# Performance work log

Measured on AMD Instinct MI355X. Metric: run time of the kernel, lower is better.

Reference implementation:

```python
import jax, jax.numpy as jnp
import numpy as np

KERNEL_SIZE = 3  # matches init kwarg

def setup_inputs() -> dict:
    key = jax.random.key(0)
    k1, k2, k3, k4 = jax.random.split(key, 4)
    N, C, L, OUT = 32, 64, 2048, 128
    inp = jax.random.normal(k1, (N, C, L), dtype=jnp.float32)
    # adjacency-like dense matrix (tree adjacency may be sparse; dense here)
    m = jax.random.uniform(k2, (N, L, L), dtype=jnp.float32)
    W = jax.random.normal(k3, (OUT, KERNEL_SIZE * C), dtype=jnp.float32) * 0.05
    b = jax.random.normal(k4, (OUT,), dtype=jnp.float32)
    return {"input": inp, "m": m, "W": W, "b": b}

def reference(input, m, W, b):
    # propagate features over the tree adjacency kernel_size-1 times
    ys = [input]
    y = input
    for _ in range(KERNEL_SIZE - 1):
        y = jnp.matmul(y, m)          # (N, C, L) @ (N, L, L) -> (N, C, L)
        ys.append(y)
    cat = jnp.concatenate(ys, axis=1)  # (N, k*C, L)
    # 1x1 conv == channel projection
    out = jnp.einsum('oc,ncl->nol', W, cat) + b[None, :, None]
    return out
```

## Files before the change

kernel.cpp:

```cpp
#include <hip/hip_runtime.h>
#include <hip/hip_bf16.h>

#define NB   32
#define CH   64
#define LL   2048
#define OUTC 128

typedef float  f32x4  __attribute__((ext_vector_type(4)));
typedef short  s16x8  __attribute__((ext_vector_type(8)));
typedef short  s16x4  __attribute__((ext_vector_type(4)));
typedef unsigned short u16;

__device__ __forceinline__ u16 f2bf(float f) {
  unsigned int u = __builtin_bit_cast(unsigned int, f);
  u += 0x7FFFu + ((u >> 16) & 1u);
  return (u16)(u >> 16);
}

__device__ __forceinline__ s16x8 pack8c(const float* v) {
  s16x8 r;
#pragma unroll
  for (int j = 0; j < 8; j += 2) {
    __hip_bfloat162 h = __float22bfloat162_rn(make_float2(v[j], v[j + 1]));
    short2 s;
    __builtin_memcpy(&s, &h, sizeof(s));
    r[j] = s.x; r[j + 1] = s.y;
  }
  return r;
}

__device__ __forceinline__ s16x4 pack4c(const f32x4& v) {
  s16x4 r;
  __hip_bfloat162 h0 = __float22bfloat162_rn(make_float2(v[0], v[1]));
  __hip_bfloat162 h1 = __float22bfloat162_rn(make_float2(v[2], v[3]));
  short2 s0, s1;
  __builtin_memcpy(&s0, &h0, sizeof(s0));
  __builtin_memcpy(&s1, &h1, sizeof(s1));
  r[0] = s0.x; r[1] = s0.y; r[2] = s1.x; r[3] = s1.y;
  return r;
}

#define NX (NB * CH * LL)
#define NW (OUTC * 3 * CH)
__global__ __launch_bounds__(256)
void cvt_inputs(const float* __restrict__ x, const float* __restrict__ W,
                u16* __restrict__ xb, u16* __restrict__ Wb)
{
  const size_t t8 = ((size_t)blockIdx.x * 256 + threadIdx.x) * 8;
  if (t8 < NX) {
    float v[8];
    *(f32x4*)(v)     = *(const f32x4*)(x + t8);
    *(f32x4*)(v + 4) = *(const f32x4*)(x + t8 + 4);
    *(s16x8*)(xb + t8) = pack8c(v);
  } else if (t8 - NX < NW) {
    const size_t w8 = t8 - NX;
    float v[8];
    *(f32x4*)(v)     = *(const f32x4*)(W + w8);
    *(f32x4*)(v + 4) = *(const f32x4*)(W + w8 + 4);
    *(s16x8*)(Wb + w8) = pack8c(v);
  }
}

__global__ __launch_bounds__(256, 2)
void prop1_pack(const u16* __restrict__ xb, const float* __restrict__ m,
                u16* __restrict__ y1, u16* __restrict__ mP)
{
  __shared__ float smem[4][32 * 128];

  const int n    = blockIdx.x >> 4;
  const int lt   = blockIdx.x & 15;
  const int tid  = threadIdx.x;
  const int wave = tid >> 6;
  const int lane = tid & 63;
  const int l15  = lane & 15;
  const int g4   = lane >> 4;
  const int colb = lt * 128 + wave * 32;

  const float* mn   = m + (size_t)n * LL * LL + lt * 128;
  const float* gsrc = mn + (size_t)(wave * 8 + (lane >> 5)) * LL + (lane & 31) * 4;
  const u16*   ap   = xb + (size_t)n * CH * LL + (size_t)l15 * LL + g4 * 8;
  u16* q0 = mP + (((size_t)n * 64 * LL + colb + l15) * 4 + g4) * 8;
  u16* o  = y1 + (size_t)n * CH * LL + colb + l15;

  f32x4 acc[4][2];
#pragma unroll
  for (int f = 0; f < 4; ++f)
#pragma unroll
    for (int h = 0; h < 2; ++h)
#pragma unroll
      for (int r = 0; r < 4; ++r) acc[f][h][r] = 0.f;

  s16x8 aP[4], aQ[4];

#define ALOAD(R, KB)                                                          \
  { const u16* _ap = ap + (KB) * 32;                                          \
    _Pragma("unroll") for (int f = 0; f < 4; ++f)                             \
      R[f] = *(const s16x8*)(_ap + (size_t)(f * 16) * LL); }

#define GLOAD(BI, KB)                                                         \
  { float* _sb = smem[BI];                                                    \
    _Pragma("unroll") for (int i = 0; i < 4; ++i) {                           \
      const float* _g = gsrc + (size_t)((KB) * 32 + i * 2) * LL;              \
      __builtin_amdgcn_global_load_lds(                                       \
        (const __attribute__((address_space(1))) void*)_g,                    \
        (__attribute__((address_space(3))) void*)(_sb + (wave * 4 + i) * 256),\
        16, 0, 0); } }

  ALOAD(aP, 0)
  __builtin_amdgcn_sched_barrier(0);
  GLOAD(0, 0) GLOAD(1, 1) GLOAD(2, 2)
  __builtin_amdgcn_sched_barrier(0);
  asm volatile("s_waitcnt vmcnt(8)" ::: "memory");
  __builtin_amdgcn_s_barrier();
  __builtin_amdgcn_sched_barrier(0);

#define K1_STEP(KB, CUR, NXT, VN, LAST)                                       \
  {                                                                           \
    if (!(LAST)) {                                                            \
      ALOAD(NXT, ((KB) + 1 < 64 ? (KB) + 1 : 63))                             \
      __builtin_amdgcn_sched_barrier(0);                                      \
      GLOAD(((KB) + 3) & 3, ((KB) + 3 < 64 ? (KB) + 3 : 63))                  \
      __builtin_amdgcn_sched_barrier(0);                                      \
    }                                                                         \
    const float* _t = smem[(KB) & 3] + wave * 32 + l15;                       \
    float _bv0[8], _bv1[8];                                                   \
    _Pragma("unroll") for (int j = 0; j < 8; ++j) {                           \
      _bv0[j] = _t[(g4 * 8 + j) * 128];                                       \
      _bv1[j] = _t[(g4 * 8 + j) * 128 + 16];                                  \
    }                                                                         \
    s16x8 _b0 = pack8c(_bv0), _b1 = pack8c(_bv1);                             \
    u16* _q = q0 + (size_t)(KB) * 65536;                                      \
    *(s16x8*)(_q)       = _b0;                                                \
    *(s16x8*)(_q + 512) = _b1;                                                \
    _Pragma("unroll") for (int f = 0; f < 4; ++f) {                           \
      acc[f][0] = __builtin_amdgcn_mfma_f32_16x16x32_bf16(CUR[f], _b0, acc[f][0], 0, 0, 0); \
      acc[f][1] = __builtin_amdgcn_mfma_f32_16x16x32_bf16(CUR[f], _b1, acc[f][1], 0, 0, 0); \
    }                                                                         \
    if (!(LAST)) {                                                            \
      __builtin_amdgcn_sched_barrier(0);                                      \
      asm volatile("s_waitcnt vmcnt(" VN ")" ::: "memory");                   \
      __builtin_amdgcn_s_barrier();                                           \
      __builtin_amdgcn_sched_barrier(0);                                      \
    }                                                                         \
  }

  K1_STEP(0, aP, aQ, "14", false)
  K1_STEP(1, aQ, aP, "20", false)
#pragma unroll 1
  for (int kb = 2; kb < 62; kb += 2) {
    K1_STEP(kb,     aP, aQ, "22", false)
    K1_STEP(kb + 1, aQ, aP, "22", false)
  }
  K1_STEP(62, aP, aQ, "22", false)
  K1_STEP(63, aQ, aP, "0",  true)

#pragma unroll
  for (int f = 0; f < 4; ++f)
#pragma unroll
    for (int r = 0; r < 4; ++r) {
      const int row = f * 16 + g4 * 4 + r;
      o[(size_t)row * LL]      = f2bf(acc[f][0][r]);
      o[(size_t)row * LL + 16] = f2bf(acc[f][1][r]);
    }
}

__global__ __launch_bounds__(256, 2)
void prop2_proj(const u16* __restrict__ y1, const u16* __restrict__ mP,
                const u16* __restrict__ xb, const u16* __restrict__ Wb,
                const float* __restrict__ bias, float* __restrict__ out)
{
  __shared__ u16 yT[128 * 72];

  const int n    = blockIdx.x >> 4;
  const int lt   = blockIdx.x & 15;
  const int tid  = threadIdx.x;
  const int wave = tid >> 6;
  const int lane = tid & 63;
  const int l15  = lane & 15;
  const int g4   = lane >> 4;
  const int colb = lt * 128 + wave * 32;

  const u16* mq = mP + (((size_t)n * 64 * LL + colb + l15) * 4 + g4) * 8;
  const u16* ap = y1 + (size_t)n * CH * LL + (size_t)l15 * LL + g4 * 8;

  f32x4 acc[4][2];
#pragma unroll
  for (int f = 0; f < 4; ++f)
#pragma unroll
    for (int h = 0; h < 2; ++h)
#pragma unroll
      for (int r = 0; r < 4; ++r) acc[f][h][r] = 0.f;

  s16x8 bA0, bA1, bB0, bB1, aA[4], aB[4];

#define K2_LOAD(B0, B1, AV, KB)                                              \
  {                                                                          \
    const u16* _mq = mq + (size_t)(KB) * 65536;                              \
    B0 = *(const s16x8*)(_mq);                                               \
    B1 = *(const s16x8*)(_mq + 512);                                         \
    const u16* _ap = ap + (KB) * 32;                                         \
    _Pragma("unroll") for (int f = 0; f < 4; ++f)                            \
      AV[f] = *(const s16x8*)(_ap + (size_t)(f * 16) * LL);                  \
  }

#define K2_COMP(B0, B1, AV)                                                  \
  _Pragma("unroll") for (int f = 0; f < 4; ++f) {                            \
    acc[f][0] = __builtin_amdgcn_mfma_f32_16x16x32_bf16(AV[f], B0, acc[f][0], 0, 0, 0); \
    acc[f][1] = __builtin_amdgcn_mfma_f32_16x16x32_bf16(AV[f], B1, acc[f][1], 0, 0, 0); \
  }

  K2_LOAD(bA0, bA1, aA, 0)
#pragma unroll 1
  for (int kb = 0; kb < 64; kb += 2) {
    K2_LOAD(bB0, bB1, aB, kb + 1)
    K2_COMP(bA0, bA1, aA)
    if (kb + 2 < 64) K2_LOAD(bA0, bA1, aA, kb + 2)
    K2_COMP(bB0, bB1, aB)
  }

#pragma unroll
  for (int f = 0; f < 4; ++f)
#pragma unroll
    for (int h = 0; h < 2; ++h) {
      const int c = wave * 32 + l15 + 16 * h;
      *(s16x4*)(&yT[c * 72 + f * 16 + g4 * 4]) = pack4c(acc[f][h]);
    }
  __syncthreads();

  f32x4 acc2[8][2];
#pragma unroll
  for (int f = 0; f < 8; ++f)
#pragma unroll
    for (int h = 0; h < 2; ++h)
#pragma unroll
      for (int r = 0; r < 4; ++r) acc2[f][h][r] = 0.f;

  const size_t cb = (size_t)n * CH * LL + colb + l15;
  const u16* xp  = xb + cb + (size_t)(g4 * 8) * LL;
  const u16* y1p = y1 + cb + (size_t)(g4 * 8) * LL;
  const u16* wq  = Wb + (size_t)l15 * 192 + g4 * 8;

#pragma unroll
  for (int kc = 0; kc < 6; ++kc) {
    const int k0 = kc * 32;
    s16x8 b0, b1;
    if (kc < 4) {
      const u16* src = (kc < 2) ? (xp + (size_t)k0 * LL)
                                : (y1p + (size_t)(k0 - 64) * LL);
#pragma unroll
      for (int j = 0; j < 8; ++j) {
        b0[j] = (short)src[(size_t)j * LL];
        b1[j] = (short)src[(size_t)j * LL + 16];
      }
    } else {
      const int rb = (kc - 4) * 32 + g4 * 8;
      b0 = *(const s16x8*)(&yT[(wave * 32 + l15) * 72 + rb]);
      b1 = *(const s16x8*)(&yT[(wave * 32 + l15 + 16) * 72 + rb]);
    }
#pragma unroll
    for (int f = 0; f < 8; ++f) {
      s16x8 af = *(const s16x8*)(wq + (size_t)(f * 16) * 192 + k0);
      acc2[f][0] = __builtin_amdgcn_mfma_f32_16x16x32_bf16(af, b0, acc2[f][0], 0, 0, 0);
      acc2[f][1] = __builtin_amdgcn_mfma_f32_16x16x32_bf16(af, b1, acc2[f][1], 0, 0, 0);
    }
  }

  float* op = out + (size_t)n * OUTC * LL + colb + l15;
#pragma unroll
  for (int f = 0; f < 8; ++f)
#pragma unroll
    for (int r = 0; r < 4; ++r) {
      const int row = f * 16 + g4 * 4 + r;
      op[(size_t)row * LL]      = acc2[f][0][r] + bias[row];
      op[(size_t)row * LL + 16] = acc2[f][1][r] + bias[row];
    }
}

extern "C" void kernel_launch(void* const* d_in, const int* in_sizes, int n_in,
                              void* d_out, int out_size, void* d_ws, size_t ws_size,
                              hipStream_t stream)
{
  const float* x = (const float*)d_in[0];
  const float* m = (const float*)d_in[1];
  const float* W = (const float*)d_in[2];
  const float* b = (const float*)d_in[3];
  float* out = (float*)d_out;

  u16* y1 = (u16*)d_ws;
  u16* xb = y1 + (size_t)NB * CH * LL;
  u16* Wb = xb + (size_t)NB * CH * LL;
  u16* mP = (u16*)((char*)d_ws + (25u << 20));

  cvt_inputs<<<dim3(2060), dim3(256), 0, stream>>>(x, W, xb, Wb);
  prop1_pack<<<dim3(NB * 16), dim3(256), 0, stream>>>(xb, m, y1, mP);
  prop2_proj<<<dim3(NB * 16), dim3(256), 0, stream>>>(y1, mP, xb, Wb, b, out);
}
```

Baseline: 271.6 us.

## Split propagation kernels into single-wave blocks and drop workgroup barriers

Both propagation kernels now launch 64-thread, single-wave blocks over a grid four times larger. Each wave owns a 32-column tile with its own small LDS ring, so the per-step s_barrier and __syncthreads go away and waits use only vmcnt. The second kernel also moves from double to triple register buffering of its global loads, keeping more memory requests in flight. In exchange, the hand-tuned vmcnt values must now match the new per-step load and store counts exactly, and there are more, smaller blocks to schedule.

```diff
diff --git a/kernel.cpp b/kernel.cpp
--- a/kernel.cpp
+++ b/kernel.cpp
@@ -61,23 +61,21 @@
   }
 }
 
-__global__ __launch_bounds__(256, 2)
+__global__ __launch_bounds__(64)
 void prop1_pack(const u16* __restrict__ xb, const float* __restrict__ m,
                 u16* __restrict__ y1, u16* __restrict__ mP)
 {
-  __shared__ float smem[4][32 * 128];
-
-  const int n    = blockIdx.x >> 4;
-  const int lt   = blockIdx.x & 15;
-  const int tid  = threadIdx.x;
-  const int wave = tid >> 6;
-  const int lane = tid & 63;
+  __shared__ float smem[4][32 * 32];
+
+  const int n    = blockIdx.x >> 6;
+  const int lt   = blockIdx.x & 63;
+  const int lane = threadIdx.x;
   const int l15  = lane & 15;
   const int g4   = lane >> 4;
-  const int colb = lt * 128 + wave * 32;
-
-  const float* mn   = m + (size_t)n * LL * LL + lt * 128;
-  const float* gsrc = mn + (size_t)(wave * 8 + (lane >> 5)) * LL + (lane & 31) * 4;
+  const int colb = lt * 32;
+
+  const float* mn   = m + (size_t)n * LL * LL + colb;
+  const float* gsrc = mn + (size_t)(lane >> 3) * LL + (lane & 7) * 4;
   const u16*   ap   = xb + (size_t)n * CH * LL + (size_t)l15 * LL + g4 * 8;
   u16* q0 = mP + (((size_t)n * 64 * LL + colb + l15) * 4 + g4) * 8;
   u16* o  = y1 + (size_t)n * CH * LL + colb + l15;
@@ -100,18 +98,15 @@
 #define GLOAD(BI, KB)                                                         \
   { float* _sb = smem[BI];                                                    \
     _Pragma("unroll") for (int i = 0; i < 4; ++i) {                           \
-      const float* _g = gsrc + (size_t)((KB) * 32 + i * 2) * LL;              \
+      const float* _g = gsrc + (size_t)((KB) * 32 + i * 8) * LL;              \
       __builtin_amdgcn_global_load_lds(                                       \
         (const __attribute__((address_space(1))) void*)_g,                    \
-        (__attribute__((address_space(3))) void*)(_sb + (wave * 4 + i) * 256),\
+        (__attribute__((address_space(3))) void*)(_sb + i * 256),             \
         16, 0, 0); } }
 
   ALOAD(aP, 0)
   __builtin_amdgcn_sched_barrier(0);
   GLOAD(0, 0) GLOAD(1, 1) GLOAD(2, 2)
-  __builtin_amdgcn_sched_barrier(0);
-  asm volatile("s_waitcnt vmcnt(8)" ::: "memory");
-  __builtin_amdgcn_s_barrier();
   __builtin_amdgcn_sched_barrier(0);
 
 #define K1_STEP(KB, CUR, NXT, VN, LAST)                                       \
@@ -122,11 +117,13 @@
       GLOAD(((KB) + 3) & 3, ((KB) + 3 < 64 ? (KB) + 3 : 63))                  \
       __builtin_amdgcn_sched_barrier(0);                                      \
     }                                                                         \
-    const float* _t = smem[(KB) & 3] + wave * 32 + l15;                       \
+    asm volatile("s_waitcnt vmcnt(" VN ")" ::: "memory");                     \
+    __builtin_amdgcn_sched_barrier(0);                                        \
+    const float* _t = smem[(KB) & 3] + l15;                                   \
     float _bv0[8], _bv1[8];                                                   \
     _Pragma("unroll") for (int j = 0; j < 8; ++j) {                           \
-      _bv0[j] = _t[(g4 * 8 + j) * 128];                                       \
-      _bv1[j] = _t[(g4 * 8 + j) * 128 + 16];                                  \
+      _bv0[j] = _t[(g4 * 8 + j) * 32];                                        \
+      _bv1[j] = _t[(g4 * 8 + j) * 32 + 16];                                   \
     }                                                                         \
     s16x8 _b0 = pack8c(_bv0), _b1 = pack8c(_bv1);                             \
     u16* _q = q0 + (size_t)(KB) * 65536;                                      \
@@ -136,23 +133,17 @@
       acc[f][0] = __builtin_amdgcn_mfma_f32_16x16x32_bf16(CUR[f], _b0, acc[f][0], 0, 0, 0); \
       acc[f][1] = __builtin_amdgcn_mfma_f32_16x16x32_bf16(CUR[f], _b1, acc[f][1], 0, 0, 0); \
     }                                                                         \
-    if (!(LAST)) {                                                            \
-      __builtin_amdgcn_sched_barrier(0);                                      \
-      asm volatile("s_waitcnt vmcnt(" VN ")" ::: "memory");                   \
-      __builtin_amdgcn_s_barrier();                                           \
-      __builtin_amdgcn_sched_barrier(0);                                      \
-    }                                                                         \
-  }
-
-  K1_STEP(0, aP, aQ, "14", false)
-  K1_STEP(1, aQ, aP, "20", false)
+  }
+
+  K1_STEP(0, aP, aQ, "16", false)
+  K1_STEP(1, aQ, aP, "22", false)
+  K1_STEP(2, aP, aQ, "28", false)
 #pragma unroll 1
-  for (int kb = 2; kb < 62; kb += 2) {
-    K1_STEP(kb,     aP, aQ, "22", false)
-    K1_STEP(kb + 1, aQ, aP, "22", false)
-  }
-  K1_STEP(62, aP, aQ, "22", false)
-  K1_STEP(63, aQ, aP, "0",  true)
+  for (int kb = 3; kb < 63; kb += 2) {
+    K1_STEP(kb,     aQ, aP, "30", false)
+    K1_STEP(kb + 1, aP, aQ, "30", false)
+  }
+  K1_STEP(63, aQ, aP, "22", true)
 
 #pragma unroll
   for (int f = 0; f < 4; ++f)
@@ -164,21 +155,19 @@
     }
 }
 
-__global__ __launch_bounds__(256, 2)
+__global__ __launch_bounds__(64)
 void prop2_proj(const u16* __restrict__ y1, const u16* __restrict__ mP,
                 const u16* __restrict__ xb, const u16* __restrict__ Wb,
                 const float* __restrict__ bias, float* __restrict__ out)
 {
-  __shared__ u16 yT[128 * 72];
-
-  const int n    = blockIdx.x >> 4;
-  const int lt   = blockIdx.x & 15;
-  const int tid  = threadIdx.x;
-  const int wave = tid >> 6;
-  const int lane = tid & 63;
+  __shared__ u16 yT[32 * 72];
+
+  const int n    = blockIdx.x >> 6;
+  const int lt   = blockIdx.x & 63;
+  const int lane = threadIdx.x;
   const int l15  = lane & 15;
   const int g4   = lane >> 4;
-  const int colb = lt * 128 + wave * 32;
+  const int colb = lt * 32;
 
   const u16* mq = mP + (((size_t)n * 64 * LL + colb + l15) * 4 + g4) * 8;
   const u16* ap = y1 + (size_t)n * CH * LL + (size_t)l15 * LL + g4 * 8;
@@ -191,7 +180,7 @@
 #pragma unroll
       for (int r = 0; r < 4; ++r) acc[f][h][r] = 0.f;
 
-  s16x8 bA0, bA1, bB0, bB1, aA[4], aB[4];
+  s16x8 bA0, bA1, aA[4], bB0, bB1, aB[4], bC0, bC1, aC[4];
 
 #define K2_LOAD(B0, B1, AV, KB)                                              \
   {                                                                          \
@@ -210,22 +199,26 @@
   }
 
   K2_LOAD(bA0, bA1, aA, 0)
+  K2_LOAD(bB0, bB1, aB, 1)
+  K2_LOAD(bC0, bC1, aC, 2)
 #pragma unroll 1
-  for (int kb = 0; kb < 64; kb += 2) {
-    K2_LOAD(bB0, bB1, aB, kb + 1)
+  for (int kb = 0; kb < 63; kb += 3) {
     K2_COMP(bA0, bA1, aA)
-    if (kb + 2 < 64) K2_LOAD(bA0, bA1, aA, kb + 2)
+    K2_LOAD(bA0, bA1, aA, (kb + 3 < 64 ? kb + 3 : 63))
     K2_COMP(bB0, bB1, aB)
-  }
+    K2_LOAD(bB0, bB1, aB, (kb + 4 < 64 ? kb + 4 : 63))
+    K2_COMP(bC0, bC1, aC)
+    K2_LOAD(bC0, bC1, aC, (kb + 5 < 64 ? kb + 5 : 63))
+  }
+  K2_COMP(bA0, bA1, aA)
 
 #pragma unroll
   for (int f = 0; f < 4; ++f)
 #pragma unroll
     for (int h = 0; h < 2; ++h) {
-      const int c = wave * 32 + l15 + 16 * h;
+      const int c = l15 + 16 * h;
       *(s16x4*)(&yT[c * 72 + f * 16 + g4 * 4]) = pack4c(acc[f][h]);
     }
-  __syncthreads();
 
   f32x4 acc2[8][2];
 #pragma unroll
@@ -254,8 +247,8 @@
       }
     } else {
       const int rb = (kc - 4) * 32 + g4 * 8;
-      b0 = *(const s16x8*)(&yT[(wave * 32 + l15) * 72 + rb]);
-      b1 = *(const s16x8*)(&yT[(wave * 32 + l15 + 16) * 72 + rb]);
+      b0 = *(const s16x8*)(&yT[l15 * 72 + rb]);
+      b1 = *(const s16x8*)(&yT[(l15 + 16) * 72 + rb]);
     }
 #pragma unroll
     for (int f = 0; f < 8; ++f) {
@@ -292,6 +285,6 @@
   u16* mP = (u16*)((char*)d_ws + (25u << 20));
 
   cvt_inputs<<<dim3(2060), dim3(256), 0, stream>>>(x, W, xb, Wb);
-  prop1_pack<<<dim3(NB * 16), dim3(256), 0, stream>>>(xb, m, y1, mP);
-  prop2_proj<<<dim3(NB * 16), dim3(256), 0, stream>>>(y1, mP, xb, Wb, b, out);
-}
+  prop1_pack<<<dim3(NB * 64), dim3(64), 0, stream>>>(xb, m, y1, mP);
+  prop2_proj<<<dim3(NB * 64), dim3(64), 0, stream>>>(y1, mP, xb, Wb, b, out);
+}
```

Result: slower. 326.2 us (+20.1%).
